# Kernel optimization log

Measured on AMD Instinct MI355X. Metric: run time of the kernel, lower is better.

The kernel has to match this reference:

```python
import jax, jax.numpy as jnp
import numpy as np

HID = 5120       # hidden_size
H = 32           # num_heads (TP shard)
Q_RANK = 1536    # q_lora_rank
KV_RANK = 512    # kv_lora_rank
D_NOPE = 128     # qk_nope_head_dim
D_ROPE = 64      # qk_rope_head_dim
DV = 128         # v_head_dim
Q_HEAD = D_NOPE + D_ROPE
T = 2048
EPS = 1e-6
ROPE_BASE = 10000.0
SCALE = Q_HEAD ** -0.5
NEG = jnp.finfo(jnp.float32).min


def rmsnorm(x, w):
    return x * jax.lax.rsqrt(jnp.mean(x * x, axis=-1, keepdims=True) + EPS) * w


def rope(x, pos):
    # half-split (GPT-NeoX style) rotary; the torch module permutes weights in
    # _update_pe so that interleaved RoPE becomes exactly this half-split form.
    half = x.shape[-1] // 2
    inv = 1.0 / (ROPE_BASE ** (jnp.arange(half, dtype=jnp.float32) / half))
    ang = pos.astype(jnp.float32)[:, None] * inv          # [T, half]
    cos, sin = jnp.cos(ang), jnp.sin(ang)
    if x.ndim == 3:                                       # [T, H, D]
        cos, sin = cos[:, None, :], sin[:, None, :]
    x1, x2 = jnp.split(x, 2, axis=-1)
    return jnp.concatenate([x1 * cos - x2 * sin, x2 * cos + x1 * sin], axis=-1)


def setup_inputs() -> dict:
    key = jax.random.key(0)
    ks = jax.random.split(key, 10)
    s = 0.02
    return {
        'hidden_states': jax.random.normal(ks[0], (1, T, HID), jnp.float32),
        'position_ids': jnp.arange(T, dtype=jnp.int64),
        'w_q_a': jax.random.normal(ks[1], (Q_RANK, HID), jnp.float32) * s,
        'q_a_ln_w': jnp.ones((Q_RANK,), jnp.float32),
        'w_q_b': jax.random.normal(ks[2], (H * Q_HEAD, Q_RANK), jnp.float32) * s,
        'w_kv_a': jax.random.normal(ks[3], (KV_RANK + D_ROPE, HID), jnp.float32) * s,
        'kv_a_ln_w': jnp.ones((KV_RANK,), jnp.float32),
        'w_kc': jax.random.normal(ks[4], (H, D_NOPE, KV_RANK), jnp.float32) * s,
        'w_vc': jax.random.normal(ks[5], (H, KV_RANK, DV), jnp.float32) * s,
        'w_o': jax.random.normal(ks[6], (HID, H * DV), jnp.float32) * s,
    }


def reference(hidden_states, position_ids, w_q_a, q_a_ln_w, w_q_b, w_kv_a,
              kv_a_ln_w, w_kc, w_vc, w_o):
    h = hidden_states[0]                                   # [T, HID]
    t = h.shape[0]
    # q low-rank path: q_a_proj -> rmsnorm -> q_b_proj
    q = rmsnorm(h @ w_q_a.T, q_a_ln_w) @ w_q_b.T           # [T, H*Q_HEAD]
    q = q.reshape(t, H, Q_HEAD)
    q_nope, q_pe = q[..., :D_NOPE], q[..., D_NOPE:]
    # absorb kv_b (w_kc): project q into the latent kv space
    q_lat = jnp.einsum('thn,hnk->thk', q_nope, w_kc)       # [T, H, KV_RANK]
    # kv low-rank path (MQA-style shared latent)
    ckv_full = h @ w_kv_a.T                                # [T, KV_RANK+D_ROPE]
    ckv = rmsnorm(ckv_full[:, :KV_RANK], kv_a_ln_w)        # [T, KV_RANK]
    k_pe = rope(ckv_full[:, KV_RANK:], position_ids)       # [T, D_ROPE]
    q_pe = rope(q_pe, position_ids)                        # [T, H, D_ROPE]
    # full query/key in latent+pe space; key/value shared across heads
    qf = jnp.concatenate([q_lat, q_pe], axis=-1)           # [T, H, KV_RANK+D_ROPE]
    kf = jnp.concatenate([ckv, k_pe], axis=-1)             # [T, KV_RANK+D_ROPE]
    scores = jnp.einsum('thd,sd->hts', qf, kf) * SCALE     # [H, T, T]
    causal = jnp.tril(jnp.ones((t, t), dtype=bool))
    scores = jnp.where(causal[None], scores, NEG)
    p = jax.nn.softmax(scores, axis=-1)
    o = jnp.einsum('hts,sk->thk', p, ckv)                  # [T, H, KV_RANK]
    o = jnp.einsum('thk,hkv->thv', o, w_vc)                # [T, H, DV]
    out = o.reshape(t, H * DV) @ w_o.T                     # [T, HID]
    return out[None]
```

## Files before the change

### kernel.cpp

```cpp
#include <hip/hip_runtime.h>
#include <hip/hip_bf16.h>
#include <type_traits>

typedef __attribute__((ext_vector_type(8))) short short8;
typedef __attribute__((ext_vector_type(4))) float f32x4;
using bf16 = __hip_bfloat16;

#define T_SEQ 2048
#define NH 32
#define SCALE_F 0.07216878364870323f

__device__ inline unsigned short f2bf(float f) {
    unsigned u = __builtin_bit_cast(unsigned, f);
    return (unsigned short)((u + 0x7fffu + ((u >> 16) & 1u)) >> 16);
}

__device__ inline void gload_lds16(const void* g, void* l) {
    __builtin_amdgcn_global_load_lds(
        (const __attribute__((address_space(1))) unsigned*)g,
        (__attribute__((address_space(3))) unsigned*)l, 16, 0, 0);
}

template <typename TC>
__global__ __launch_bounds__(512, 2) void gemm8p_kernel(
    const bf16* __restrict__ A, const bf16* __restrict__ B, TC* __restrict__ C,
    int K, int lda, int ldb, int ldc)
{
    extern __shared__ char Lds[];
    const int bm = blockIdx.y * 256, bn = blockIdx.x * 256;
    const int tid = threadIdx.x, lane = tid & 63, w = tid >> 6;
    const int l15 = lane & 15, lg = lane >> 4;
    const int wmr = (w >> 2) * 64;
    const int wnc = (w & 3) * 32;
    const int lrh = lane >> 3;
    const int scolb = ((lane & 7) * 16) ^ ((lane >> 3) << 4);
    const int rdswz = (l15 & 7) << 4;
    const bf16* Ab = A + (long)bm * lda;
    const bf16* Bb = B + (long)bn * ldb;
    const int nt = K >> 6;

    auto stage_half = [&](int tt, int isB, int h) {
        const int buf = tt & 1;
        const int k0 = (tt >= nt ? tt - nt : tt) << 6;
        const bf16* Base = isB ? Bb : Ab;
        const int ld = isB ? ldb : lda;
        const char* g = (const char*)Base
            + ((long)(h * 128 + w * 8 + lrh) * ld + k0) * 2 + scolb;
        char* l = Lds + buf * 65536 + isB * 32768 + h * 16384 + w * 1024;
        gload_lds16(g, l);
        gload_lds16(g + (long)128 * ld, l + 8192);
    };

    f32x4 acc[4][4][2] = {};
    stage_half(0, 0, 0); stage_half(0, 1, 1); stage_half(0, 0, 1);
    stage_half(0, 1, 0); stage_half(1, 0, 0); stage_half(1, 1, 1);
    asm volatile("s_waitcnt vmcnt(4)" ::: "memory");
    __builtin_amdgcn_s_barrier();

    for (int t = 0; t < nt; ++t) {
        const char* Bufp = Lds + (t & 1) * 65536;
        short8 aF[4][2], bF[2][2];
        #define ARD(mh, fi, ks) \
            (*(const short8*)(Bufp + (mh) * 16384 + (wmr + (fi) * 16 + l15) * 128 \
                              + (((ks) * 64 + lg * 16) ^ rdswz)))
        #define BRD(nh, nj, ks) \
            (*(const short8*)(Bufp + 32768 + (nh) * 16384 + (wnc + (nj) * 16 + l15) * 128 \
                              + (((ks) * 64 + lg * 16) ^ rdswz)))
        #define MFMA16(q) \
            __builtin_amdgcn_s_setprio(1); \
            _Pragma("unroll") for (int ks = 0; ks < 2; ++ks) \
            _Pragma("unroll") for (int fi = 0; fi < 4; ++fi) \
            _Pragma("unroll") for (int nj = 0; nj < 2; ++nj) \
                acc[q][fi][nj] = __builtin_amdgcn_mfma_f32_16x16x32_bf16( \
                    aF[fi][ks], bF[nj][ks], acc[q][fi][nj], 0, 0, 0); \
            __builtin_amdgcn_s_setprio(0);

        #pragma unroll
        for (int fi = 0; fi < 4; ++fi) { aF[fi][0] = ARD(0, fi, 0); aF[fi][1] = ARD(0, fi, 1); }
        #pragma unroll
        for (int nj = 0; nj < 2; ++nj) { bF[nj][0] = BRD(0, nj, 0); bF[nj][1] = BRD(0, nj, 1); }
        stage_half(t + 1, 0, 1);
        asm volatile("s_waitcnt lgkmcnt(8)" ::: "memory");
        __builtin_amdgcn_s_barrier();
        asm volatile("s_waitcnt lgkmcnt(0)" ::: "memory");
        __builtin_amdgcn_sched_barrier(0);
        MFMA16(0)
        __builtin_amdgcn_s_barrier();
        #pragma unroll
        for (int nj = 0; nj < 2; ++nj) { bF[nj][0] = BRD(1, nj, 0); bF[nj][1] = BRD(1, nj, 1); }
        stage_half(t + 1, 1, 0);
        __builtin_amdgcn_s_barrier();
        asm volatile("s_waitcnt lgkmcnt(0)" ::: "memory");
        __builtin_amdgcn_sched_barrier(0);
        MFMA16(1)
        __builtin_amdgcn_s_barrier();
        #pragma unroll
        for (int fi = 0; fi < 4; ++fi) { aF[fi][0] = ARD(1, fi, 0); aF[fi][1] = ARD(1, fi, 1); }
        stage_half(t + 2, 0, 0);
        __builtin_amdgcn_s_barrier();
        asm volatile("s_waitcnt lgkmcnt(0)" ::: "memory");
        __builtin_amdgcn_sched_barrier(0);
        MFMA16(2)
        __builtin_amdgcn_s_barrier();
        #pragma unroll
        for (int nj = 0; nj < 2; ++nj) { bF[nj][0] = BRD(0, nj, 0); bF[nj][1] = BRD(0, nj, 1); }
        stage_half(t + 2, 1, 1);
        __builtin_amdgcn_s_barrier();
        asm volatile("s_waitcnt lgkmcnt(0)" ::: "memory");
        __builtin_amdgcn_sched_barrier(0);
        MFMA16(3)
        asm volatile("s_waitcnt vmcnt(4)" ::: "memory");
        __builtin_amdgcn_s_barrier();
        #undef ARD
        #undef BRD
        #undef MFMA16
    }
    asm volatile("s_waitcnt vmcnt(0)" ::: "memory");
    const int QMH[4] = {0, 0, 1, 1}, QNH[4] = {0, 1, 1, 0};
    #pragma unroll
    for (int q = 0; q < 4; ++q)
        #pragma unroll
        for (int fi = 0; fi < 4; ++fi)
            #pragma unroll
            for (int nj = 0; nj < 2; ++nj)
                #pragma unroll
                for (int i = 0; i < 4; ++i) {
                    const int row = bm + QMH[q] * 128 + wmr + fi * 16 + lg * 4 + i;
                    const int col = bn + QNH[q] * 128 + wnc + nj * 16 + l15;
                    if constexpr (std::is_same<TC, float>::value)
                        C[(long)row * ldc + col] = acc[q][fi][nj][i];
                    else
                        ((unsigned short*)C)[(long)row * ldc + col] = f2bf(acc[q][fi][nj][i]);
                }
}

template <typename TC>
__global__ __launch_bounds__(256, 2) void gemmhw_kernel(
    const bf16* __restrict__ A, const bf16* __restrict__ B, TC* __restrict__ C,
    int K, int lda, int ldb, int ldc,
    long aStride, long bStride, long cStride)
{
    const int z = blockIdx.z;
    A += (long)z * aStride; B += (long)z * bStride; C += (long)z * cStride;
    const int bm = blockIdx.y * 256, bn = blockIdx.x * 128;
    __shared__ __align__(16) short As[2][256 * 32];
    __shared__ __align__(16) short Bs[2][128 * 32];
    const int tid = threadIdx.x, lane = tid & 63, w = tid >> 6;
    const int l15 = lane & 15, lg = lane >> 4;
    const int wm = w >> 1, wn = w & 1;
    const int sx = (lane & 7) ^ (lane >> 3);
    const int lrh = lane >> 3;
    const int srp = sx >> 2;
    const int scol = (sx & 3) * 8;
    const bf16* Ab = A + (long)bm * lda;
    const bf16* Bb = B + (long)bn * ldb;

    auto stage = [&](int buf, int k0) {
        #pragma unroll
        for (int jj = 0; jj < 4; ++jj) {
            const int j = w * 4 + jj;
            const int srow = 2 * (j * 8 + lrh) + srp;
            gload_lds16(Ab + (long)srow * lda + k0 + scol, &As[buf][j * 512]);
        }
        #pragma unroll
        for (int jj = 0; jj < 2; ++jj) {
            const int j = w * 2 + jj;
            const int srow = 2 * (j * 8 + lrh) + srp;
            gload_lds16(Bb + (long)srow * ldb + k0 + scol, &Bs[buf][j * 512]);
        }
    };

    const int rslot = ((((l15 & 1) << 2) | lg) ^ (l15 >> 1)) << 4;
    const int lrow_lo = l15 >> 1;
    f32x4 acc[8][4] = {};
    const int nt = K >> 5;
    stage(0, 0);
    for (int t = 0; t < nt; ++t) {
        if (t + 1 < nt) {
            stage((t + 1) & 1, (t + 1) << 5);
            asm volatile("s_waitcnt vmcnt(6)" ::: "memory");
        } else {
            asm volatile("s_waitcnt vmcnt(0)" ::: "memory");
        }
        __builtin_amdgcn_s_barrier();
        __builtin_amdgcn_sched_barrier(0);
        const char* Ap = (const char*)&As[t & 1][0];
        const char* Bp = (const char*)&Bs[t & 1][0];
        short8 af[8], bf[4];
        #pragma unroll
        for (int fi = 0; fi < 8; ++fi)
            af[fi] = *(const short8*)(Ap + (wm * 64 + fi * 8 + lrow_lo) * 128 + rslot);
        #pragma unroll
        for (int nj = 0; nj < 4; ++nj)
            bf[nj] = *(const short8*)(Bp + (wn * 32 + nj * 8 + lrow_lo) * 128 + rslot);
        #pragma unroll
        for (int fi = 0; fi < 8; ++fi)
            #pragma unroll
            for (int nj = 0; nj < 4; ++nj)
                acc[fi][nj] = __builtin_amdgcn_mfma_f32_16x16x32_bf16(
                    af[fi], bf[nj], acc[fi][nj], 0, 0, 0);
        asm volatile("s_waitcnt lgkmcnt(0)" ::: "memory");
        __builtin_amdgcn_sched_barrier(0);
        __builtin_amdgcn_s_barrier();
        __builtin_amdgcn_sched_barrier(0);
    }
    #pragma unroll
    for (int fi = 0; fi < 8; ++fi)
        #pragma unroll
        for (int nj = 0; nj < 4; ++nj)
            #pragma unroll
            for (int i = 0; i < 4; ++i) {
                const int row = bm + wm * 128 + fi * 16 + lg * 4 + i;
                const int col = bn + wn * 64 + nj * 16 + l15;
                if constexpr (std::is_same<TC, float>::value)
                    C[(long)row * ldc + col] = acc[fi][nj][i];
                else
                    ((unsigned short*)C)[(long)row * ldc + col] = f2bf(acc[fi][nj][i]);
            }
}

template <typename TC>
__global__ __launch_bounds__(512, 4) void gemm8w_kernel(
    const bf16* __restrict__ A, const bf16* __restrict__ B, TC* __restrict__ C,
    int K, int lda, int ldb, int ldc,
    long aStride, long bStride, long cStride)
{
    const int z = blockIdx.z;
    A += (long)z * aStride; B += (long)z * bStride; C += (long)z * cStride;
    const int bm = blockIdx.y * 128, bn = blockIdx.x * 128;
    __shared__ __align__(16) short As[2][128 * 64];
    __shared__ __align__(16) short Bs[2][128 * 64];
    const int tid = threadIdx.x, lane = tid & 63, w = tid >> 6;
    const int l15 = lane & 15, lg = lane >> 4;
    const int wm = w >> 1, wn = w & 1;
    const int c0 = w * 2, c1 = w * 2 + 1;
    const int srow0 = c0 * 8 + (lane >> 3), srow1 = c1 * 8 + (lane >> 3);
    const int scol = ((lane & 7) * 16) ^ ((lane >> 3) << 4);
    const bf16* Ab = A + (long)bm * lda;
    const bf16* Bb = B + (long)bn * ldb;

    auto stage = [&](int buf, int k0) {
        const char* ag = (const char*)(Ab + k0);
        const char* bg = (const char*)(Bb + k0);
        gload_lds16(ag + (long)srow0 * (lda * 2) + scol, &As[buf][c0 * 512]);
        gload_lds16(ag + (long)srow1 * (lda * 2) + scol, &As[buf][c1 * 512]);
        gload_lds16(bg + (long)srow0 * (ldb * 2) + scol, &Bs[buf][c0 * 512]);
        gload_lds16(bg + (long)srow1 * (ldb * 2) + scol, &Bs[buf][c1 * 512]);
    };

    const int swz = (l15 & 7) << 4;
    f32x4 acc[2][4] = {};
    const int nt = K >> 6;
    stage(0, 0);
    for (int t = 0; t < nt; ++t) {
        if (t + 1 < nt) {
            stage((t + 1) & 1, (t + 1) << 6);
            asm volatile("s_waitcnt vmcnt(4)" ::: "memory");
        } else {
            asm volatile("s_waitcnt vmcnt(0)" ::: "memory");
        }
        __builtin_amdgcn_s_barrier();
        __builtin_amdgcn_sched_barrier(0);
        const char* Ap = (const char*)&As[t & 1][0];
        const char* Bp = (const char*)&Bs[t & 1][0];
        short8 af[2][2], bfv[4][2];
        #pragma unroll
        for (int fi = 0; fi < 2; ++fi)
            #pragma unroll
            for (int ks = 0; ks < 2; ++ks)
                af[fi][ks] = *(const short8*)(Ap + (wm * 32 + fi * 16 + l15) * 128
                                              + ((ks * 64 + lg * 16) ^ swz));
        #pragma unroll
        for (int nj = 0; nj < 4; ++nj)
            #pragma unroll
            for (int ks = 0; ks < 2; ++ks)
                bfv[nj][ks] = *(const short8*)(Bp + (wn * 64 + nj * 16 + l15) * 128
                                               + ((ks * 64 + lg * 16) ^ swz));
        #pragma unroll
        for (int ks = 0; ks < 2; ++ks)
            #pragma unroll
            for (int fi = 0; fi < 2; ++fi)
                #pragma unroll
                for (int nj = 0; nj < 4; ++nj)
                    acc[fi][nj] = __builtin_amdgcn_mfma_f32_16x16x32_bf16(
                        af[fi][ks], bfv[nj][ks], acc[fi][nj], 0, 0, 0);
        asm volatile("s_waitcnt lgkmcnt(0)" ::: "memory");
        __builtin_amdgcn_sched_barrier(0);
        __builtin_amdgcn_s_barrier();
        __builtin_amdgcn_sched_barrier(0);
    }
    #pragma unroll
    for (int fi = 0; fi < 2; ++fi)
        #pragma unroll
        for (int nj = 0; nj < 4; ++nj)
            #pragma unroll
            for (int i = 0; i < 4; ++i) {
                const int row = bm + wm * 32 + fi * 16 + lg * 4 + i;
                const int col = bn + wn * 64 + nj * 16 + l15;
                if constexpr (std::is_same<TC, float>::value)
                    C[(long)row * ldc + col] = acc[fi][nj][i];
                else
                    ((unsigned short*)C)[(long)row * ldc + col] = f2bf(acc[fi][nj][i]);
            }
}

__global__ __launch_bounds__(256) void cvt_kernel(
    const float* __restrict__ in, bf16* __restrict__ out, long n, float scale)
{
    const long i = ((long)blockIdx.x * 256 + threadIdx.x) * 8;
    if (i >= n) return;
    f32x4 a = *(const f32x4*)(in + i), b = *(const f32x4*)(in + i + 4);
    short8 r;
    r[0] = (short)f2bf(a[0] * scale); r[1] = (short)f2bf(a[1] * scale);
    r[2] = (short)f2bf(a[2] * scale); r[3] = (short)f2bf(a[3] * scale);
    r[4] = (short)f2bf(b[0] * scale); r[5] = (short)f2bf(b[1] * scale);
    r[6] = (short)f2bf(b[2] * scale); r[7] = (short)f2bf(b[3] * scale);
    *(short8*)(out + i) = r;
}

__global__ __launch_bounds__(256) void tconv_kernel(
    const float* __restrict__ in, bf16* __restrict__ out)
{
    const int h = blockIdx.z, k0 = blockIdx.x * 32, d0 = blockIdx.y * 32;
    __shared__ float t[32][33];
    const int r = threadIdx.x >> 5, c = threadIdx.x & 31;
    const float* ip = in + ((long)h * 512 + k0) * 128 + d0;
    #pragma unroll
    for (int it = 0; it < 4; ++it)
        t[r + 8 * it][c] = ip[(long)(r + 8 * it) * 128 + c];
    __syncthreads();
    bf16* op = out + ((long)h * 128 + d0) * 512 + k0;
    #pragma unroll
    for (int it = 0; it < 4; ++it)
        op[(long)(r + 8 * it) * 512 + c] = __float2bfloat16(t[c][r + 8 * it]);
}

__global__ __launch_bounds__(256) void rmsnorm_kernel(
    bf16* __restrict__ x, const float* __restrict__ w, int C, int ld)
{
    bf16* row = x + (long)blockIdx.x * ld;
    float ss = 0.f;
    for (int i = threadIdx.x; i < C; i += 256) {
        float v = __bfloat162float(row[i]);
        ss += v * v;
    }
    #pragma unroll
    for (int m = 1; m < 64; m <<= 1) ss += __shfl_xor(ss, m, 64);
    __shared__ float red[4];
    if ((threadIdx.x & 63) == 0) red[threadIdx.x >> 6] = ss;
    __syncthreads();
    ss = red[0] + red[1] + red[2] + red[3];
    float scale = rsqrtf(ss / (float)C + 1e-6f);
    for (int i = threadIdx.x; i < C; i += 256) {
        float v = __bfloat162float(row[i]);
        row[i] = __float2bfloat16(v * scale * w[i]);
    }
}

__global__ __launch_bounds__(256) void ropeq_kernel(bf16* __restrict__ q)
{
    const int t = blockIdx.x;
    #pragma unroll
    for (int it = 0; it < 4; ++it) {
        const int pair = threadIdx.x + 256 * it;
        const int h = pair >> 5, i = pair & 31;
        bf16* base = q + ((long)t * NH + h) * 192;
        float x1 = __bfloat162float(base[128 + i]);
        float x2 = __bfloat162float(base[160 + i]);
        float inv = powf(10000.f, -(float)i / 32.f);
        float ang = (float)t * inv, s, c;
        sincosf(ang, &s, &c);
        base[128 + i] = __float2bfloat16(x1 * c - x2 * s);
        base[160 + i] = __float2bfloat16(x2 * c + x1 * s);
    }
}

__global__ __launch_bounds__(1024) void ropek_kernel(
    const bf16* __restrict__ ckv, bf16* __restrict__ kf, int ld)
{
    const int t = blockIdx.x;
    const int h = threadIdx.x >> 5, i = threadIdx.x & 31;
    float x1 = __bfloat162float(ckv[(long)t * ld + 512 + i]);
    float x2 = __bfloat162float(ckv[(long)t * ld + 544 + i]);
    float inv = powf(10000.f, -(float)i / 32.f);
    float ang = (float)t * inv, s, c;
    sincosf(ang, &s, &c);
    bf16* kb = kf + ((long)h * T_SEQ + t) * 192;
    kb[128 + i] = __float2bfloat16(x1 * c - x2 * s);
    kb[160 + i] = __float2bfloat16(x2 * c + x1 * s);
}

__global__ __launch_bounds__(256, 2) void attn_kernel(
    const bf16* __restrict__ Q,
    const bf16* __restrict__ Kf,
    const bf16* __restrict__ Vt,
    bf16* __restrict__ O)
{
    const int lin = blockIdx.x;
    const int h = (lin & 7) + 8 * ((lin >> 3) & 3);
    const int qraw = lin >> 5;
    const int qblk = (qraw < 8) ? (2 * qraw) : (31 - 2 * qraw);
    const int q0 = qblk * 128;
    const int tid = threadIdx.x, lane = tid & 63, w = tid >> 6;
    const int l15 = lane & 15, lg = lane >> 4;
    const int qw = q0 + w * 32;
    __shared__ __align__(16) short Ks[2][64 * 192];
    __shared__ __align__(16) short Vs[2][128 * 64];

    int ksoff[6];
    #pragma unroll
    for (int j = 0; j < 6; ++j) {
        int o = (w * 6 + j) * 1024 + lane * 16;
        int row = o / 384, col = o % 384;
        ksoff[j] = row * 384 + (col ^ ((row & 7) << 4));
    }
    const int vrow8 = lane >> 3;
    const int vscol = ((lane & 7) * 16) ^ (vrow8 << 4);

    short8 qf[2][6];
    #pragma unroll
    for (int qi = 0; qi < 2; ++qi) {
        const bf16* qp = Q + (long)(qw + qi * 16 + l15) * (NH * 192) + (long)h * 192;
        #pragma unroll
        for (int c = 0; c < 6; ++c) qf[qi][c] = *(const short8*)(qp + c * 32 + lg * 8);
    }

    f32x4 oacc[2][8] = {};
    float mst[2] = {-INFINITY, -INFINITY};
    float lst[2] = {0.f, 0.f};

    const char* kbase0 = (const char*)Kf + (long)h * T_SEQ * 384;
    const char* vbase0 = (const char*)Vt + (long)h * 128 * (T_SEQ * 2);
    const int swz = (l15 & 7) << 4;
    const int nt = (q0 + 128) >> 6;

    auto stage = [&](int t) {
        char* KsB = (char*)&Ks[t & 1][0];
        char* VsB = (char*)&Vs[t & 1][0];
        const char* kb = kbase0 + (long)(t * 64) * 384;
        #pragma unroll
        for (int j = 0; j < 6; ++j)
            gload_lds16(kb + ksoff[j], KsB + (w * 6 + j) * 1024);
        const char* vb = vbase0 + (long)(t * 64) * 2 + vscol;
        #pragma unroll
        for (int j = 0; j < 4; ++j) {
            const int c = w * 4 + j;
            gload_lds16(vb + (long)(c * 8 + vrow8) * (T_SEQ * 2), VsB + c * 1024);
        }
    };

    stage(0);
    for (int t = 0; t < nt; ++t) {
        const int s0 = t * 64;
        if (t + 1 < nt) {
            stage(t + 1);
            asm volatile("s_waitcnt vmcnt(10)" ::: "memory");
        } else {
            asm volatile("s_waitcnt vmcnt(0)" ::: "memory");
        }
        __builtin_amdgcn_s_barrier();
        __builtin_amdgcn_sched_barrier(0);
        if (s0 <= qw + 31) {
            const char* KsB = (const char*)&Ks[t & 1][0];
            const char* VsB = (const char*)&Vs[t & 1][0];
            f32x4 st[2][4] = {};
            __builtin_amdgcn_s_setprio(1);
            #pragma unroll
            for (int cb = 0; cb < 4; ++cb) {
                const int krow = cb * 16 + l15;
                #pragma unroll
                for (int c = 0; c < 6; ++c) {
                    short8 kfr = *(const short8*)(KsB + krow * 384
                                                  + ((c * 64 + lg * 16) ^ swz));
                    st[0][cb] = __builtin_amdgcn_mfma_f32_16x16x32_bf16(kfr, qf[0][c], st[0][cb], 0, 0, 0);
                    st[1][cb] = __builtin_amdgcn_mfma_f32_16x16x32_bf16(kfr, qf[1][c], st[1][cb], 0, 0, 0);
                }
            }
            __builtin_amdgcn_s_setprio(0);
            short8 pb[2][2];
            #pragma unroll
            for (int qi = 0; qi < 2; ++qi) {
                const int qg = qw + qi * 16 + l15;
                float pmax = -INFINITY;
                #pragma unroll
                for (int cb = 0; cb < 4; ++cb)
                    #pragma unroll
                    for (int i = 0; i < 4; ++i) {
                        const int kv = s0 + cb * 16 + lg * 4 + i;
                        float v = (kv <= qg) ? st[qi][cb][i] : -INFINITY;
                        st[qi][cb][i] = v;
                        pmax = fmaxf(pmax, v);
                    }
                pmax = fmaxf(pmax, __shfl_xor(pmax, 16, 64));
                pmax = fmaxf(pmax, __shfl_xor(pmax, 32, 64));
                const float newm = fmaxf(mst[qi], pmax);
                const float mm = (newm == -INFINITY) ? 0.f : newm;
                const float alpha = __expf(mst[qi] - mm);
                float ps = 0.f;
                #pragma unroll
                for (int cb = 0; cb < 4; ++cb)
                    #pragma unroll
                    for (int i = 0; i < 4; ++i) {
                        const float e = __expf(st[qi][cb][i] - mm);
                        st[qi][cb][i] = e; ps += e;
                    }
                ps += __shfl_xor(ps, 16, 64);
                ps += __shfl_xor(ps, 32, 64);
                lst[qi] = lst[qi] * alpha + ps;
                mst[qi] = newm;
                #pragma unroll
                for (int mb = 0; mb < 8; ++mb) oacc[qi][mb] *= alpha;
                #pragma unroll
                for (int hh = 0; hh < 2; ++hh) {
                    unsigned pk[4];
                    #pragma unroll
                    for (int i = 0; i < 4; ++i)
                        pk[i] = (unsigned)f2bf(st[qi][2 * hh][i])
                              | ((unsigned)f2bf(st[qi][2 * hh + 1][i]) << 16);
                    #pragma unroll
                    for (int j = 0; j < 8; ++j) {
                        const int src = l15 + (((2 * lg + (j >> 2)) & 3) << 4);
                        const unsigned u = (unsigned)__shfl((int)pk[j & 3], src, 64);
                        pb[qi][hh][j] = (short)((lg >> 1) ? (u >> 16) : (u & 0xffffu));
                    }
                }
            }
            __builtin_amdgcn_s_setprio(1);
            #pragma unroll
            for (int mb = 0; mb < 8; ++mb) {
                const int vrow = mb * 16 + l15;
                #pragma unroll
                for (int hh = 0; hh < 2; ++hh) {
                    short8 vfr = *(const short8*)(VsB + vrow * 128
                                                  + ((hh * 64 + lg * 16) ^ swz));
                    oacc[0][mb] = __builtin_amdgcn_mfma_f32_16x16x32_bf16(vfr, pb[0][hh], oacc[0][mb], 0, 0, 0);
                    oacc[1][mb] = __builtin_amdgcn_mfma_f32_16x16x32_bf16(vfr, pb[1][hh], oacc[1][mb], 0, 0, 0);
                }
            }
            __builtin_amdgcn_s_setprio(0);
        }
        __builtin_amdgcn_sched_barrier(0);
        __builtin_amdgcn_s_barrier();
    }
    #pragma unroll
    for (int qi = 0; qi < 2; ++qi) {
        const float inv = 1.f / lst[qi];
        const int qg = qw + qi * 16 + l15;
        #pragma unroll
        for (int mb = 0; mb < 8; ++mb)
            #pragma unroll
            for (int i = 0; i < 4; ++i) {
                const int dv = mb * 16 + lg * 4 + i;
                O[(long)qg * (NH * 128) + h * 128 + dv] = __float2bfloat16(oacc[qi][mb][i] * inv);
            }
    }
}

extern "C" void kernel_launch(void* const* d_in, const int* in_sizes, int n_in,
                              void* d_out, int out_size, void* d_ws, size_t ws_size,
                              hipStream_t stream)
{
    const float* hidden    = (const float*)d_in[0];
    const float* w_q_a     = (const float*)d_in[2];
    const float* q_a_ln_w  = (const float*)d_in[3];
    const float* w_q_b     = (const float*)d_in[4];
    const float* w_kv_a    = (const float*)d_in[5];
    const float* kv_a_ln_w = (const float*)d_in[6];
    const float* w_kc      = (const float*)d_in[7];
    const float* w_vc      = (const float*)d_in[8];
    const float* w_o       = (const float*)d_in[9];
    float* out = (float*)d_out;

    bf16* qckv  = (bf16*)d_ws;
    bf16* qbuf  = qckv  + (long)T_SEQ * 2176;
    bf16* kf    = qbuf  + (long)T_SEQ * 6144;
    bf16* vt    = kf    + (long)NH * T_SEQ * 192;
    bf16* ov    = vt    + (long)NH * 128 * T_SEQ;
    bf16* hb    = ov    + (long)T_SEQ * 4096;
    bf16* wqckv = hb    + (long)T_SEQ * 5120;
    bf16* wqb   = wqckv + (long)2176 * 5120;
    bf16* wkc   = wqb   + (long)6144 * 1536;
    bf16* wvct  = wkc   + (long)NH * 128 * 512;
    bf16* wo    = hb;
    bf16* ckv   = qckv + 1536;

    cvt_kernel<<<dim3(5120), 256, 0, stream>>>(hidden, hb, (long)T_SEQ * 5120, 1.f);
    cvt_kernel<<<dim3(3840), 256, 0, stream>>>(w_q_a, wqckv, (long)1536 * 5120, 1.f);
    cvt_kernel<<<dim3(1440), 256, 0, stream>>>(w_kv_a, wqckv + (long)1536 * 5120,
                                               (long)576 * 5120, 1.f);
    hipMemsetAsync(wqckv + (long)2112 * 5120, 0, (long)64 * 5120 * sizeof(bf16), stream);
    cvt_kernel<<<dim3(4608), 256, 0, stream>>>(w_q_b, wqb, (long)6144 * 1536, SCALE_F);
    cvt_kernel<<<dim3(1024), 256, 0, stream>>>(w_kc, wkc, (long)NH * 128 * 512, 1.f);
    tconv_kernel<<<dim3(16, 4, NH), 256, 0, stream>>>(w_vc, wvct);

    gemm8w_kernel<bf16><<<dim3(17, 16, 1), 512, 0, stream>>>(
        hb, wqckv, qckv, 5120, 5120, 5120, 2176, 0, 0, 0);
    rmsnorm_kernel<<<dim3(T_SEQ), 256, 0, stream>>>(qckv, q_a_ln_w, 1536, 2176);
    rmsnorm_kernel<<<dim3(T_SEQ), 256, 0, stream>>>(ckv, kv_a_ln_w, 512, 2176);
    gemm8p_kernel<bf16><<<dim3(24, 8), 512, 131072, stream>>>(
        qckv, wqb, qbuf, 1536, 2176, 1536, 6144);
    ropeq_kernel<<<dim3(T_SEQ), 256, 0, stream>>>(qbuf);
    ropek_kernel<<<dim3(T_SEQ), 1024, 0, stream>>>(ckv, kf, 2176);
    gemmhw_kernel<bf16><<<dim3(1, 8, NH), 256, 0, stream>>>(
        ckv, wkc, kf, 512, 2176, 512, 192,
        0, (long)128 * 512, (long)T_SEQ * 192);
    gemm8p_kernel<bf16><<<dim3(8, 16), 512, 131072, stream>>>(
        wvct, ckv, vt, 512, 512, 2176, 2048);
    cvt_kernel<<<dim3(10240), 256, 0, stream>>>(w_o, wo, (long)5120 * 4096, 1.f);
    attn_kernel<<<dim3(512), 256, 0, stream>>>(qbuf, kf, vt, ov);
    gemm8p_kernel<float><<<dim3(20, 8), 512, 131072, stream>>>(
        ov, wo, out, 4096, 4096, 4096, 5120);
}
```

Baseline: 463.6 us.

## Swizzle GEMM tiles, fold w_o conversion into attention, lazy softmax rescale

The two GEMM kernels remap their linear block index so consecutive workgroups are spread across XCD-style groups of eight, aiming for better L2 locality. The separate w_o fp32-to-bf16 conversion launch is merged into the attention kernel as extra blocks beyond index 512, so the conversion fills idle CUs during attention and one launch is saved. The online softmax now skips the running-max update and output rescale unless some row's new max exceeds the stored max by more than 8, which cuts exp and multiply work per tile. Deferred rescaling lets exponentials reach up to e^8 before renormalising, which stays within fp32 range but slightly loosens bf16 precision of P.

```diff
diff --git a/kernel.cpp b/kernel.cpp
--- a/kernel.cpp
+++ b/kernel.cpp
@@ -27,7 +27,10 @@
     int K, int lda, int ldb, int ldc)
 {
     extern __shared__ char Lds[];
-    const int bm = blockIdx.y * 256, bn = blockIdx.x * 256;
+    const int nwg = gridDim.x * gridDim.y;
+    const int lin = blockIdx.y * gridDim.x + blockIdx.x;
+    const int lin2 = (lin & 7) * (nwg >> 3) + (lin >> 3);
+    const int bm = (lin2 / gridDim.x) * 256, bn = (lin2 % gridDim.x) * 256;
     const int tid = threadIdx.x, lane = tid & 63, w = tid >> 6;
     const int l15 = lane & 15, lg = lane >> 4;
     const int wmr = (w >> 2) * 64;
@@ -227,7 +230,10 @@
 {
     const int z = blockIdx.z;
     A += (long)z * aStride; B += (long)z * bStride; C += (long)z * cStride;
-    const int bm = blockIdx.y * 128, bn = blockIdx.x * 128;
+    const int nwg = gridDim.x * gridDim.y;
+    const int lin = blockIdx.y * gridDim.x + blockIdx.x;
+    const int lin2 = (lin & 7) * (nwg >> 3) + (lin >> 3);
+    const int bm = (lin2 / gridDim.x) * 128, bn = (lin2 % gridDim.x) * 128;
     __shared__ __align__(16) short As[2][128 * 64];
     __shared__ __align__(16) short Bs[2][128 * 64];
     const int tid = threadIdx.x, lane = tid & 63, w = tid >> 6;
@@ -394,8 +400,24 @@
     const bf16* __restrict__ Q,
     const bf16* __restrict__ Kf,
     const bf16* __restrict__ Vt,
-    bf16* __restrict__ O)
-{
+    bf16* __restrict__ O,
+    const float* __restrict__ WOin, bf16* __restrict__ WOout)
+{
+    if (blockIdx.x >= 512) {
+        const long base = ((long)blockIdx.x - 512) * 16384 + threadIdx.x * 8;
+        #pragma unroll
+        for (int it = 0; it < 8; ++it) {
+            const long i = base + (long)it * 2048;
+            f32x4 a = *(const f32x4*)(WOin + i), b = *(const f32x4*)(WOin + i + 4);
+            short8 r;
+            r[0] = (short)f2bf(a[0]); r[1] = (short)f2bf(a[1]);
+            r[2] = (short)f2bf(a[2]); r[3] = (short)f2bf(a[3]);
+            r[4] = (short)f2bf(b[0]); r[5] = (short)f2bf(b[1]);
+            r[6] = (short)f2bf(b[2]); r[7] = (short)f2bf(b[3]);
+            *(short8*)(WOout + i) = r;
+        }
+        return;
+    }
     const int lin = blockIdx.x;
     const int h = (lin & 7) + 8 * ((lin >> 3) & 3);
     const int qraw = lin >> 5;
@@ -477,7 +499,7 @@
                 }
             }
             __builtin_amdgcn_s_setprio(0);
-            short8 pb[2][2];
+            float pmaxv[2];
             #pragma unroll
             for (int qi = 0; qi < 2; ++qi) {
                 const int qg = qw + qi * 16 + l15;
@@ -493,9 +515,25 @@
                     }
                 pmax = fmaxf(pmax, __shfl_xor(pmax, 16, 64));
                 pmax = fmaxf(pmax, __shfl_xor(pmax, 32, 64));
-                const float newm = fmaxf(mst[qi], pmax);
-                const float mm = (newm == -INFINITY) ? 0.f : newm;
-                const float alpha = __expf(mst[qi] - mm);
+                pmaxv[qi] = pmax;
+            }
+            const bool full = !__all((pmaxv[0] - mst[0] <= 8.f) &&
+                                     (pmaxv[1] - mst[1] <= 8.f));
+            short8 pb[2][2];
+            #pragma unroll
+            for (int qi = 0; qi < 2; ++qi) {
+                float mm;
+                if (full) {
+                    const float newm = fmaxf(mst[qi], pmaxv[qi]);
+                    mm = (newm == -INFINITY) ? 0.f : newm;
+                    const float alpha = __expf(mst[qi] - mm);
+                    lst[qi] *= alpha;
+                    mst[qi] = newm;
+                    #pragma unroll
+                    for (int mb = 0; mb < 8; ++mb) oacc[qi][mb] *= alpha;
+                } else {
+                    mm = mst[qi];
+                }
                 float ps = 0.f;
                 #pragma unroll
                 for (int cb = 0; cb < 4; ++cb)
@@ -506,10 +544,7 @@
                     }
                 ps += __shfl_xor(ps, 16, 64);
                 ps += __shfl_xor(ps, 32, 64);
-                lst[qi] = lst[qi] * alpha + ps;
-                mst[qi] = newm;
-                #pragma unroll
-                for (int mb = 0; mb < 8; ++mb) oacc[qi][mb] *= alpha;
+                lst[qi] += ps;
                 #pragma unroll
                 for (int hh = 0; hh < 2; ++hh) {
                     unsigned pk[4];
@@ -606,8 +641,7 @@
         0, (long)128 * 512, (long)T_SEQ * 192);
     gemm8p_kernel<bf16><<<dim3(8, 16), 512, 131072, stream>>>(
         wvct, ckv, vt, 512, 512, 2176, 2048);
-    cvt_kernel<<<dim3(10240), 256, 0, stream>>>(w_o, wo, (long)5120 * 4096, 1.f);
-    attn_kernel<<<dim3(512), 256, 0, stream>>>(qbuf, kf, vt, ov);
+    attn_kernel<<<dim3(1792), 256, 0, stream>>>(qbuf, kf, vt, ov, w_o, wo);
     gemm8p_kernel<float><<<dim3(20, 8), 512, 131072, stream>>>(
         ov, wo, out, 4096, 4096, 4096, 5120);
 }
```

Measured after the change: 447.0 us. 1.04x faster.
